# Performance work log

Hardware: AMD Instinct MI355X
Metric: run time of the kernel (lower is better)

The kernel has to match this reference:

```python
import jax, jax.numpy as jnp
import numpy as np

N_FFT = 2048
STRIDE = 512
PAD = N_FFT // 2  # center padding removed at the end
B = 4
T = 512  # number of spectrogram frames


def _make_kernels():
    n = np.arange(N_FFT)
    # ang[out_sample, freq_bin] = 2*pi*n*k/N  (create_fourier_kernels, freq_scale='no', freq_bins=n_fft)
    ang = 2.0 * np.pi * np.outer(n, n) / N_FFT
    kernel_cos = np.cos(ang).astype(np.float32)
    kernel_sin = np.sin(ang).astype(np.float32)
    # scipy.signal.get_window('hann', N, fftbins=True) -> periodic hann
    window = (0.5 - 0.5 * np.cos(2.0 * np.pi * n / N_FFT)).astype(np.float32)
    return kernel_cos, kernel_sin, window


def setup_inputs() -> dict:
    key = jax.random.key(0)
    X = jax.random.normal(key, (B, N_FFT, T, 2), dtype=jnp.float32)
    kc, ks, w = _make_kernels()
    return {
        "X": X,
        "kernel_cos": jnp.asarray(kc),
        "kernel_sin": jnp.asarray(ks),
        "window": jnp.asarray(w),
    }


def reference(X, kernel_cos, kernel_sin, window):
    # X: (B, n_fft, T, 2) complex spectrogram (onesided=False)
    b, n_fft, t, _ = X.shape
    Xr = X[..., 0]
    Xi = X[..., 1]
    # inverse DFT via dense matmul against sinusoidal kernels (conv2d in torch):
    # frames[b, n, t] = sum_f Xr[b,f,t]*cos(2pi n f/N) - Xi[b,f,t]*sin(2pi n f/N)
    frames = (jnp.einsum('bft,nf->bnt', Xr, kernel_cos)
              - jnp.einsum('bft,nf->bnt', Xi, kernel_sin))
    frames = frames * window[None, :, None] / n_fft
    # overlap-add (torch fold): out[b, t*stride + n] += frames[b, n, t]
    out_len = n_fft + STRIDE * (t - 1)
    idx = (jnp.arange(n_fft)[:, None] + STRIDE * jnp.arange(t)[None, :]).reshape(-1)
    y = jnp.zeros((b, out_len), frames.dtype).at[:, idx].add(frames.reshape(b, -1))
    # window sum-square normalization (torch_window_sumsquare)
    w_sq = jnp.broadcast_to((window * window)[:, None], (n_fft, t)).reshape(-1)
    w_sum = jnp.zeros((out_len,), window.dtype).at[idx].add(w_sq)
    nonzero = w_sum > 1e-10
    denom = jnp.where(nonzero, w_sum, jnp.ones_like(w_sum))
    y = jnp.where(nonzero[None, :], y / denom[None, :], y)
    # center=True, length=None -> trim pad_amount from both ends
    return y[:, PAD:-PAD]
```

## Files before the change

kernel.cpp:

```cpp
#include <hip/hip_runtime.h>

#define TT   512
#define BB   4
#define OUTL 261632

typedef __attribute__((ext_vector_type(8))) short short8;
typedef __attribute__((ext_vector_type(4))) float f32x4;

__device__ __forceinline__ unsigned short f2bf(float x) {
    union { float f; unsigned int u; } v; v.f = x;
    unsigned int r = v.u + 0x7fffu + ((v.u >> 16) & 1u);
    return (unsigned short)(r >> 16);
}
__device__ __forceinline__ unsigned int pack2(float lo, float hi) {
    return ((unsigned int)f2bf(hi) << 16) | (unsigned int)f2bf(lo);
}
__device__ __forceinline__ short8 ld8(const unsigned int* p) {
    return *reinterpret_cast<const short8*>(p);
}
__device__ __forceinline__ short8 mk8(unsigned int a, unsigned int b,
                                      unsigned int c, unsigned int d) {
    union { uint4 u; short8 s; } v; v.u = make_uint4(a, b, c, d); return v.s;
}

__global__ __launch_bounds__(256) void istft_k(const float* __restrict__ X,
                                               const float* __restrict__ win,
                                               float* __restrict__ out) {
    __shared__ unsigned int B2s[4096];
    __shared__ unsigned int tile[8192];

    const int S  = blockIdx.x;
    const int L  = ((S & 7) << 6) | (S >> 3);
    const int c0 = L * 4;
    const int b  = c0 >> 9;
    const int t0 = c0 & 511;
    const int tid = threadIdx.x;
    const int w = tid >> 6, l = tid & 63;
    const int sI = l & 15, h = l >> 4;

    #pragma unroll
    for (int q = 0; q < 8; q++) {
        int i = q * 256 + tid;
        int n = i >> 5, j = i & 31, n2b = n & 31;
        float ang = (float)((n2b * j) & 31) * 0.19634954084936207f;
        float co = __cosf(ang), si = __sinf(ang);
        tile[n * 32 + j] = (n < 32) ? pack2(co, -si) : pack2(si, co);
    }
    #pragma unroll
    for (int q = 0; q < 16; q++) {
        int i = q * 256 + tid;
        int n1 = i >> 6, f1 = i & 63;
        float ang = (float)((n1 * f1) & 63) * 0.09817477042468103f;
        B2s[n1 * 64 + f1] = pack2(__cosf(ang), -__sinf(ang));
    }
    __syncthreads();

    short8 bf[4][2], b2r[4][4];
    #pragma unroll
    for (int ni = 0; ni < 4; ni++) {
        #pragma unroll
        for (int kk = 0; kk < 2; kk++)
            bf[ni][kk] = ld8(&tile[(16 * ni + sI) * 32 + 16 * kk + 4 * h]);
        #pragma unroll
        for (int kk = 0; kk < 4; kk++)
            b2r[ni][kk] = ld8(&B2s[(16 * ni + sI) * 64 + 16 * kk + 4 * h]);
    }
    __syncthreads();

    const float* Xb = X + ((size_t)(b * 2048) * 512 + t0) * 2;
    #pragma unroll
    for (int it = 0; it < 16; it++) {
        int idx = it * 256 + tid;
        int f = idx >> 1, q = idx & 1;
        float4 v = *reinterpret_cast<const float4*>(Xb + ((size_t)f * 512 + 2 * q) * 2);
        tile[f * 4 + ((2 * q + f) & 3)]     = pack2(v.x, v.y);
        tile[f * 4 + ((2 * q + 1 + f) & 3)] = pack2(v.z, v.w);
    }
    __syncthreads();

    const int slot = (w + sI) & 3;
    f32x4 acc[4][4] = {};
    #pragma unroll
    for (int mi = 0; mi < 4; mi++) {
        int f1 = 16 * mi + sI;
        short8 af[2];
        #pragma unroll
        for (int kk = 0; kk < 2; kk++) {
            int f2b = 16 * kk + 4 * h;
            af[kk] = mk8(tile[(f1 + 64 * (f2b + 0)) * 4 + slot],
                         tile[(f1 + 64 * (f2b + 1)) * 4 + slot],
                         tile[(f1 + 64 * (f2b + 2)) * 4 + slot],
                         tile[(f1 + 64 * (f2b + 3)) * 4 + slot]);
        }
        #pragma unroll
        for (int ni = 0; ni < 4; ni++)
            #pragma unroll
            for (int kk = 0; kk < 2; kk++)
                acc[mi][ni] = __builtin_amdgcn_mfma_f32_16x16x32_bf16(
                    af[kk], bf[ni][kk], acc[mi][ni], 0, 0, 0);
    }
    __syncthreads();

    f32x4 acc2[2][4] = {};
    #pragma unroll
    for (int mi2 = 0; mi2 < 2; mi2++) {
        const int n2 = 16 * mi2 + sI;
        #pragma unroll
        for (int kk = 0; kk < 4; kk++) {
            unsigned int u0, u1, u2, u3;
            #pragma unroll
            for (int j = 0; j < 4; j++) {
                int f1 = 16 * kk + 4 * h + j;
                float Gre = acc[kk][mi2][j];
                float Gim = acc[kk][mi2 + 2][j];
                float ang = (float)((n2 * f1) & 2047) * 0.0030679615757712823f;
                float co = __cosf(ang), si = __sinf(ang);
                unsigned int pv = pack2(Gre * co - Gim * si, Gre * si + Gim * co);
                if (j == 0) u0 = pv; else if (j == 1) u1 = pv;
                else if (j == 2) u2 = pv; else u3 = pv;
            }
            short8 a2f = mk8(u0, u1, u2, u3);
            #pragma unroll
            for (int ni = 0; ni < 4; ni++)
                acc2[mi2][ni] = __builtin_amdgcn_mfma_f32_16x16x32_bf16(
                    a2f, b2r[ni][kk], acc2[mi2][ni], 0, 0, 0);
        }
    }

    unsigned int* fw = tile + w * 1024;
    #pragma unroll
    for (int mi2 = 0; mi2 < 2; mi2++)
        #pragma unroll
        for (int ni = 0; ni < 4; ni++) {
            int n1 = 16 * ni + sI;
            #pragma unroll
            for (int rp = 0; rp < 2; rp++) {
                int n2a = 16 * mi2 + 4 * h + 2 * rp;
                int na  = n2a + 32 * n1;
                float w0 = 0.5f - 0.5f * __cosf((float)na * 0.0030679615757712823f);
                float w1 = 0.5f - 0.5f * __cosf((float)(na + 1) * 0.0030679615757712823f);
                fw[(n2a >> 1) + 16 * n1] =
                    pack2(acc2[mi2][ni][2 * rp] * w0, acc2[mi2][ni][2 * rp + 1] * w1);
            }
        }
    __syncthreads();

    const bool interior = (t0 >= 3) && (t0 <= 505);
    float invw0 = 0.f, invw1 = 0.f;
    {
        float s0 = 0.f, s1 = 0.f;
        #pragma unroll
        for (int k = 0; k < 4; k++) {
            float a = win[tid + 512 * k];
            float c = win[tid + 256 + 512 * k];
            s0 += a * a; s1 += c * c;
        }
        invw0 = 1.0f / (2048.0f * s0);
        invw1 = 1.0f / (2048.0f * s1);
    }
    float* outb = out + (size_t)b * OUTL;
    #pragma unroll 1
    for (int qi = 0; qi < 14; qi++) {
        int jl = tid + 256 * qi;
        int tb_l = jl >> 9, rr = jl & 511;
        float sum = 0.f;
        #pragma unroll
        for (int k = 0; k < 4; k++) {
            int m = tb_l - k;
            if (m >= 0 && m < 4) {
                int n = rr + (k << 9);
                unsigned int v = tile[m * 1024 + (n >> 1)];
                union { unsigned int u; float f; } cv;
                cv.u = ((n & 1) ? (v >> 16) : (v & 0xffffu)) << 16;
                sum += cv.f;
            }
        }
        int j  = t0 * 512 + jl;
        int jp = j - 1024;
        if (jp < 0 || jp >= OUTL) continue;
        float y;
        if (interior) {
            y = sum * ((qi & 1) ? invw1 : invw0);
        } else {
            int tb = j >> 9;
            float s = 0.f;
            #pragma unroll
            for (int k = 0; k < 4; k++) {
                int t = tb - k;
                if (t >= 0 && t < TT) { float ww = win[rr + (k << 9)]; s += ww * ww; }
            }
            y = sum * (1.0f / 2048.0f);
            if (s > 1e-10f) y /= s;
        }
        if (jl >= 1536 && jl < 2048) outb[jp] = y;
        else                         atomicAdd(outb + jp, y);
    }
}

extern "C" void kernel_launch(void* const* d_in, const int* in_sizes, int n_in,
                              void* d_out, int out_size, void* d_ws, size_t ws_size,
                              hipStream_t stream) {
    const float* X  = (const float*)d_in[0];
    const float* w  = (const float*)d_in[3];
    float* out = (float*)d_out;

    hipMemsetAsync(out, 0, (size_t)out_size * sizeof(float), stream);
    istft_k<<<dim3(BB * TT / 4), dim3(256), 0, stream>>>(X, w, out);
}
```

Baseline: 29.67 us.

## Precompute twiddle tables in prep kernel and fuse DFT stages per k-slice

Moves the per-block construction of the two small DFT twiddle tables into a separate prep kernel that writes them to workspace, so each main block reads them from global memory or cache instead of computing sin/cos into shared memory. The first- and second-stage MFMA loops are interleaved per k-slice, so only four stage-one accumulators are live at once rather than sixteen, and B2s shared memory is dropped. Launch bounds now request higher occupancy. In exchange, B operands are reloaded from global memory inside the loop and an extra kernel launch is added, which can add latency.

```diff
diff --git a/kernel.cpp b/kernel.cpp
--- a/kernel.cpp
+++ b/kernel.cpp
@@ -23,10 +23,28 @@
     union { uint4 u; short8 s; } v; v.u = make_uint4(a, b, c, d); return v.s;
 }
 
-__global__ __launch_bounds__(256) void istft_k(const float* __restrict__ X,
-                                               const float* __restrict__ win,
-                                               float* __restrict__ out) {
-    __shared__ unsigned int B2s[4096];
+__global__ __launch_bounds__(256) void prep_k(unsigned int* __restrict__ B1g,
+                                              unsigned int* __restrict__ B2g) {
+    int tid = blockIdx.x * 256 + threadIdx.x;
+    if (tid < 2048) {
+        int n = tid >> 5, j = tid & 31, n2b = n & 31;
+        float ang = (float)((n2b * j) & 31) * 0.19634954084936207f;
+        float co = __cosf(ang), si = __sinf(ang);
+        B1g[n * 32 + j] = (n < 32) ? pack2(co, -si) : pack2(si, co);
+    }
+    int t2 = tid - 2048;
+    if (t2 >= 0 && t2 < 4096) {
+        int n1 = t2 >> 6, f1 = t2 & 63;
+        float ang = (float)((n1 * f1) & 63) * 0.09817477042468103f;
+        B2g[n1 * 64 + f1] = pack2(__cosf(ang), -__sinf(ang));
+    }
+}
+
+__global__ __launch_bounds__(256, 4) void istft_k(const float* __restrict__ X,
+                                                  const unsigned int* __restrict__ B1g,
+                                                  const unsigned int* __restrict__ B2g,
+                                                  const float* __restrict__ win,
+                                                  float* __restrict__ out) {
     __shared__ unsigned int tile[8192];
 
     const int S  = blockIdx.x;
@@ -38,35 +56,6 @@
     const int w = tid >> 6, l = tid & 63;
     const int sI = l & 15, h = l >> 4;
 
-    #pragma unroll
-    for (int q = 0; q < 8; q++) {
-        int i = q * 256 + tid;
-        int n = i >> 5, j = i & 31, n2b = n & 31;
-        float ang = (float)((n2b * j) & 31) * 0.19634954084936207f;
-        float co = __cosf(ang), si = __sinf(ang);
-        tile[n * 32 + j] = (n < 32) ? pack2(co, -si) : pack2(si, co);
-    }
-    #pragma unroll
-    for (int q = 0; q < 16; q++) {
-        int i = q * 256 + tid;
-        int n1 = i >> 6, f1 = i & 63;
-        float ang = (float)((n1 * f1) & 63) * 0.09817477042468103f;
-        B2s[n1 * 64 + f1] = pack2(__cosf(ang), -__sinf(ang));
-    }
-    __syncthreads();
-
-    short8 bf[4][2], b2r[4][4];
-    #pragma unroll
-    for (int ni = 0; ni < 4; ni++) {
-        #pragma unroll
-        for (int kk = 0; kk < 2; kk++)
-            bf[ni][kk] = ld8(&tile[(16 * ni + sI) * 32 + 16 * kk + 4 * h]);
-        #pragma unroll
-        for (int kk = 0; kk < 4; kk++)
-            b2r[ni][kk] = ld8(&B2s[(16 * ni + sI) * 64 + 16 * kk + 4 * h]);
-    }
-    __syncthreads();
-
     const float* Xb = X + ((size_t)(b * 2048) * 512 + t0) * 2;
     #pragma unroll
     for (int it = 0; it < 16; it++) {
@@ -79,40 +68,36 @@
     __syncthreads();
 
     const int slot = (w + sI) & 3;
-    f32x4 acc[4][4] = {};
-    #pragma unroll
-    for (int mi = 0; mi < 4; mi++) {
-        int f1 = 16 * mi + sI;
-        short8 af[2];
-        #pragma unroll
-        for (int kk = 0; kk < 2; kk++) {
-            int f2b = 16 * kk + 4 * h;
-            af[kk] = mk8(tile[(f1 + 64 * (f2b + 0)) * 4 + slot],
-                         tile[(f1 + 64 * (f2b + 1)) * 4 + slot],
-                         tile[(f1 + 64 * (f2b + 2)) * 4 + slot],
-                         tile[(f1 + 64 * (f2b + 3)) * 4 + slot]);
-        }
-        #pragma unroll
-        for (int ni = 0; ni < 4; ni++)
-            #pragma unroll
-            for (int kk = 0; kk < 2; kk++)
-                acc[mi][ni] = __builtin_amdgcn_mfma_f32_16x16x32_bf16(
-                    af[kk], bf[ni][kk], acc[mi][ni], 0, 0, 0);
-    }
-    __syncthreads();
-
     f32x4 acc2[2][4] = {};
     #pragma unroll
-    for (int mi2 = 0; mi2 < 2; mi2++) {
-        const int n2 = 16 * mi2 + sI;
-        #pragma unroll
-        for (int kk = 0; kk < 4; kk++) {
+    for (int kk = 0; kk < 4; kk++) {
+        int f1r = 16 * kk + sI;
+        short8 af[2];
+        #pragma unroll
+        for (int k1 = 0; k1 < 2; k1++) {
+            int f2b = 16 * k1 + 4 * h;
+            af[k1] = mk8(tile[(f1r + 64 * (f2b + 0)) * 4 + slot],
+                         tile[(f1r + 64 * (f2b + 1)) * 4 + slot],
+                         tile[(f1r + 64 * (f2b + 2)) * 4 + slot],
+                         tile[(f1r + 64 * (f2b + 3)) * 4 + slot]);
+        }
+        f32x4 acck[4] = {};
+        #pragma unroll
+        for (int ni = 0; ni < 4; ni++)
+            #pragma unroll
+            for (int k1 = 0; k1 < 2; k1++)
+                acck[ni] = __builtin_amdgcn_mfma_f32_16x16x32_bf16(
+                    af[k1], ld8(&B1g[(16 * ni + sI) * 32 + 16 * k1 + 4 * h]),
+                    acck[ni], 0, 0, 0);
+        #pragma unroll
+        for (int mi2 = 0; mi2 < 2; mi2++) {
+            const int n2 = 16 * mi2 + sI;
             unsigned int u0, u1, u2, u3;
             #pragma unroll
             for (int j = 0; j < 4; j++) {
                 int f1 = 16 * kk + 4 * h + j;
-                float Gre = acc[kk][mi2][j];
-                float Gim = acc[kk][mi2 + 2][j];
+                float Gre = acck[mi2][j];
+                float Gim = acck[mi2 + 2][j];
                 float ang = (float)((n2 * f1) & 2047) * 0.0030679615757712823f;
                 float co = __cosf(ang), si = __sinf(ang);
                 unsigned int pv = pack2(Gre * co - Gim * si, Gre * si + Gim * co);
@@ -123,9 +108,11 @@
             #pragma unroll
             for (int ni = 0; ni < 4; ni++)
                 acc2[mi2][ni] = __builtin_amdgcn_mfma_f32_16x16x32_bf16(
-                    a2f, b2r[ni][kk], acc2[mi2][ni], 0, 0, 0);
-        }
-    }
+                    a2f, ld8(&B2g[(16 * ni + sI) * 64 + 16 * kk + 4 * h]),
+                    acc2[mi2][ni], 0, 0, 0);
+        }
+    }
+    __syncthreads();
 
     unsigned int* fw = tile + w * 1024;
     #pragma unroll
@@ -204,6 +191,10 @@
     const float* w  = (const float*)d_in[3];
     float* out = (float*)d_out;
 
+    unsigned int* B1g = (unsigned int*)d_ws;
+    unsigned int* B2g = B1g + 2048;
+
     hipMemsetAsync(out, 0, (size_t)out_size * sizeof(float), stream);
-    istft_k<<<dim3(BB * TT / 4), dim3(256), 0, stream>>>(X, w, out);
-}
+    prep_k<<<dim3(24), dim3(256), 0, stream>>>(B1g, B2g);
+    istft_k<<<dim3(BB * TT / 4), dim3(256), 0, stream>>>(X, B1g, B2g, w, out);
+}
```

New measurement: 33.12 us. 11.6% more time.
